# Optimization experiments

Measured on AMD Instinct MI355X. Metric: run time of the kernel, lower is better.

Reference implementation:

```python
import jax, jax.numpy as jnp
import numpy as np


def apply_rotary_emb(x, freqs_cis):
    # x: [B, N, H, Dh], freqs_cis: [N, Dh//2, 2]
    B, N, H, Dh = x.shape
    x2 = x.reshape(B, N, H, Dh // 2, 2)
    f = freqs_cis[None, :, None]  # [1, N, 1, Dh//2, 2]
    real = x2[..., 0] * f[..., 0] - x2[..., 1] * f[..., 1]
    imag = x2[..., 1] * f[..., 0] + x2[..., 0] * f[..., 1]
    out = jnp.stack([real, imag], axis=-1)
    return out.reshape(B, N, H, Dh).astype(x.dtype)


def setup_inputs() -> dict:
    key = jax.random.key(0)
    k1, k2, k3, k4 = jax.random.split(key, 4)
    B, N, dim, n_head = 2, 2048, 2048, 16
    head_dim = dim // n_head
    x = jax.random.normal(k1, (B, N, dim), dtype=jnp.float32)
    # realistic rotary freqs (cos/sin), though random also works for correctness
    pos = jnp.arange(N, dtype=jnp.float32)[:, None]
    inv_freq = 1.0 / (10000.0 ** (jnp.arange(0, head_dim, 2, dtype=jnp.float32) / head_dim))
    ang = pos * inv_freq[None, :]  # [N, Dh//2]
    freqs_cis = jnp.stack([jnp.cos(ang), jnp.sin(ang)], axis=-1)  # [N, Dh//2, 2]
    wqkv = jax.random.normal(k2, (dim, 3 * dim), dtype=jnp.float32) * (dim ** -0.5)
    wo = jax.random.normal(k3, (dim, dim), dtype=jnp.float32) * (dim ** -0.5)
    return {"x": x, "freqs_cis": freqs_cis, "wqkv": wqkv, "wo": wo}


def reference(x, freqs_cis, wqkv, wo):
    B, N, dim = x.shape
    n_head = 16
    head_dim = dim // n_head
    qkv = x @ wqkv  # [B, N, 3*dim]
    q, k, v = jnp.split(qkv, 3, axis=-1)
    q = q.reshape(B, N, n_head, head_dim)
    k = k.reshape(B, N, n_head, head_dim)
    v = v.reshape(B, N, n_head, head_dim)
    q = apply_rotary_emb(q, freqs_cis)
    k = apply_rotary_emb(k, freqs_cis)
    scale = 1.0 / jnp.sqrt(jnp.asarray(head_dim, dtype=q.dtype))
    scores = jnp.einsum('bqhd,bkhd->bhqk', q, k) * scale
    attn = jax.nn.softmax(scores, axis=-1)
    out = jnp.einsum('bhqk,bkhd->bqhd', attn, v).reshape(B, N, dim)
    return out @ wo
```

## Files before the change

kernel.cpp:

```cpp
#include <hip/hip_runtime.h>
#include <hip/hip_bf16.h>
#include <stdint.h>

typedef __attribute__((ext_vector_type(8))) short bf16x8;
typedef __attribute__((ext_vector_type(4))) float f32x4;
typedef __attribute__((ext_vector_type(4))) unsigned short u16x4;
typedef __attribute__((ext_vector_type(8))) unsigned short u16x8;

#define DEV __device__ __forceinline__

DEV unsigned short f2bf(float f) {
  union { __hip_bfloat16 h; unsigned short u; } cv;
  cv.h = __float2bfloat16(f);
  return cv.u;
}

DEV void gload_lds16(const void* g, void* l) {
  __builtin_amdgcn_global_load_lds(
      (__attribute__((address_space(1))) void*)(uintptr_t)g,
      (__attribute__((address_space(3))) void*)(uint32_t)(uintptr_t)l,
      16, 0, 0);
}

__global__ __launch_bounds__(256) void k_convert(const float* __restrict__ in,
                                                 unsigned short* __restrict__ out,
                                                 int n8) {
  int i = blockIdx.x * 256 + threadIdx.x;
  if (i >= n8) return;
  const float4* p = (const float4*)in + (size_t)i * 2;
  float4 a = p[0], b = p[1];
  u16x8 o;
  o[0] = f2bf(a.x); o[1] = f2bf(a.y); o[2] = f2bf(a.z); o[3] = f2bf(a.w);
  o[4] = f2bf(b.x); o[5] = f2bf(b.y); o[6] = f2bf(b.z); o[7] = f2bf(b.w);
  *((u16x8*)out + (size_t)i) = o;
}

__global__ __launch_bounds__(256) void k_transpose_bf16(const float* __restrict__ in,
                                                        unsigned short* __restrict__ out,
                                                        int R, int C) {
  __shared__ float tile[32][33];
  const int t = threadIdx.x;
  const int c0 = blockIdx.x * 32, r0 = blockIdx.y * 32;
  {
    int r = t >> 3, c4 = (t & 7) * 4;
    float4 v = *(const float4*)&in[(size_t)(r0 + r) * C + c0 + c4];
    tile[r][c4] = v.x; tile[r][c4 + 1] = v.y; tile[r][c4 + 2] = v.z; tile[r][c4 + 3] = v.w;
  }
  __syncthreads();
  int c = t >> 3, r4 = (t & 7) * 4;
  u16x4 o;
  o[0] = f2bf(tile[r4 + 0][c]); o[1] = f2bf(tile[r4 + 1][c]);
  o[2] = f2bf(tile[r4 + 2][c]); o[3] = f2bf(tile[r4 + 3][c]);
  *(u16x4*)&out[(size_t)(c0 + c) * R + r0 + r4] = o;
}

template <int EPI>
__global__ __launch_bounds__(256) void k_gemm(
    const unsigned short* __restrict__ A,
    const unsigned short* __restrict__ Bt,
    int Kdim, int Nn,
    float* __restrict__ Cout,
    unsigned short* __restrict__ qb,
    unsigned short* __restrict__ kb,
    unsigned short* __restrict__ vt,
    const float* __restrict__ freqs) {
  __shared__ unsigned short As[128 * 64];
  __shared__ unsigned short Bs[128 * 64];
  const int t = threadIdx.x;
  const int lane = t & 63, wid = t >> 6;
  const int l15 = lane & 15, l4 = lane >> 4;
  const int m0 = blockIdx.y * 128, n0 = blockIdx.x * 128;
  const int wr = (wid >> 1) * 64, wc = (wid & 1) * 64;

  f32x4 acc[4][4];
#pragma unroll
  for (int i = 0; i < 4; i++)
#pragma unroll
    for (int j = 0; j < 4; j++) acc[i][j] = (f32x4)0.f;

  for (int k0 = 0; k0 < Kdim; k0 += 64) {
    __syncthreads();
#pragma unroll
    for (int j = 0; j < 4; j++) {
      int slotbase = j * 256 + wid * 64;
      int slot = slotbase + lane;
      int row = slot >> 3, cc = slot & 7;
      int cg = cc ^ (row & 7);
      gload_lds16(A + (size_t)(m0 + row) * Kdim + k0 + cg * 8, &As[slotbase * 8]);
      gload_lds16(Bt + (size_t)(n0 + row) * Kdim + k0 + cg * 8, &Bs[slotbase * 8]);
    }
    __syncthreads();
#pragma unroll
    for (int kk = 0; kk < 2; kk++) {
      bf16x8 af[4], bfr[4];
#pragma unroll
      for (int mi = 0; mi < 4; mi++) {
        int row = wr + mi * 16 + l15;
        int c = (kk * 4 + l4) ^ (row & 7);
        af[mi] = *(const bf16x8*)&As[row * 64 + c * 8];
      }
#pragma unroll
      for (int ni = 0; ni < 4; ni++) {
        int row = wc + ni * 16 + l15;
        int c = (kk * 4 + l4) ^ (row & 7);
        bfr[ni] = *(const bf16x8*)&Bs[row * 64 + c * 8];
      }
#pragma unroll
      for (int mi = 0; mi < 4; mi++)
#pragma unroll
        for (int ni = 0; ni < 4; ni++)
          acc[mi][ni] = __builtin_amdgcn_mfma_f32_16x16x32_bf16(af[mi], bfr[ni],
                                                                acc[mi][ni], 0, 0, 0);
    }
  }

  if constexpr (EPI == 1) {
#pragma unroll
    for (int mi = 0; mi < 4; mi++) {
      int rowb = m0 + wr + mi * 16 + l4 * 4;
#pragma unroll
      for (int ni = 0; ni < 4; ni++) {
        int col = n0 + wc + ni * 16 + l15;
#pragma unroll
        for (int r = 0; r < 4; r++)
          Cout[(size_t)(rowb + r) * Nn + col] = acc[mi][ni][r];
      }
    }
  } else {
#pragma unroll
    for (int mi = 0; mi < 4; mi++) {
      int rowb = m0 + wr + mi * 16 + l4 * 4;
      int b = rowb >> 11;
      int tok0 = rowb & 2047;
#pragma unroll
      for (int ni = 0; ni < 4; ni++) {
        int col = n0 + wc + ni * 16 + l15;
        int sec = col >> 11;
        int h = (col >> 7) & 15;
        int dh = col & 127;
        if (sec == 2) {
          u16x4 o;
#pragma unroll
          for (int r = 0; r < 4; r++) o[r] = f2bf(acc[mi][ni][r]);
          *(u16x4*)&vt[((size_t)(b * 16 + h) * 128 + dh) * 2048 + tok0] = o;
        } else {
          unsigned short* dst = (sec == 0) ? qb : kb;
          int dh2 = dh >> 1;
          int odd = dh & 1;
#pragma unroll
          for (int r = 0; r < 4; r++) {
            float v = acc[mi][ni][r];
            float p = __shfl_xor(v, 1, 64);
            float2 cs = *(const float2*)&freqs[((size_t)(tok0 + r) * 64 + dh2) * 2];
            float o = odd ? (v * cs.x + p * cs.y) : (v * cs.x - p * cs.y);
            dst[((size_t)(b * 16 + h) * 2048 + tok0 + r) * 128 + dh] = f2bf(o);
          }
        }
      }
    }
  }
}

__global__ __launch_bounds__(256, 2) void k_attn(
    const unsigned short* __restrict__ qb,
    const unsigned short* __restrict__ kb,
    const unsigned short* __restrict__ vt,
    unsigned short* __restrict__ ao) {
  __shared__ unsigned short Ks[2][64 * 128];
  __shared__ unsigned short Vs[2][64 * 128];
  __shared__ unsigned short Ps[4][32 * 64];
  const int t = threadIdx.x;
  const int lane = t & 63, wid = t >> 6;
  const int l15 = lane & 15, l4 = lane >> 4;
  const int qt0 = blockIdx.x * 128;
  const int bh = blockIdx.y;
  const unsigned short* qbase = qb + (size_t)bh * 2048 * 128;
  const unsigned short* kbase = kb + (size_t)bh * 2048 * 128;
  const unsigned short* vbase = vt + (size_t)bh * 128 * 2048;

  bf16x8 qf[2][4];
#pragma unroll
  for (int mi = 0; mi < 2; mi++) {
    int qrow = qt0 + wid * 32 + mi * 16 + l15;
#pragma unroll
    for (int dk = 0; dk < 4; dk++)
      qf[mi][dk] = *(const bf16x8*)&qbase[(size_t)qrow * 128 + dk * 32 + l4 * 8];
  }

  f32x4 O[2][8];
#pragma unroll
  for (int mi = 0; mi < 2; mi++)
#pragma unroll
    for (int df = 0; df < 8; df++) O[mi][df] = (f32x4)0.f;
  float lsum[2][4];
#pragma unroll
  for (int mi = 0; mi < 2; mi++)
#pragma unroll
    for (int r = 0; r < 4; r++) lsum[mi][r] = 0.f;

  const float scale = 0.08838834764831845f;

  auto STAGE = [&](int kv0, int buf) {
#pragma unroll
    for (int j = 0; j < 4; j++) {
      int slotbase = j * 256 + wid * 64;
      int slot = slotbase + lane;
      int rowk = slot >> 4, ck = slot & 15;
      gload_lds16(&kbase[(size_t)(kv0 + rowk) * 128 + (ck ^ (rowk & 7)) * 8],
                  &Ks[buf][slotbase * 8]);
      int rowv = slot >> 3, cv = slot & 7;
      gload_lds16(&vbase[(size_t)rowv * 2048 + kv0 + (cv ^ (rowv & 7)) * 8],
                  &Vs[buf][slotbase * 8]);
    }
  };

  STAGE(0, 0);
  __syncthreads();

  for (int ti = 0; ti < 32; ti++) {
    const int cur = ti & 1;
    if (ti < 31) STAGE((ti + 1) * 64, cur ^ 1);

    f32x4 s[2][4];
#pragma unroll
    for (int mi = 0; mi < 2; mi++)
#pragma unroll
      for (int ni = 0; ni < 4; ni++) s[mi][ni] = (f32x4)0.f;
#pragma unroll
    for (int dk = 0; dk < 4; dk++) {
      bf16x8 kf[4];
#pragma unroll
      for (int ni = 0; ni < 4; ni++) {
        int row = ni * 16 + l15;
        int c = (dk * 4 + l4) ^ (row & 7);
        kf[ni] = *(const bf16x8*)&Ks[cur][row * 128 + c * 8];
      }
#pragma unroll
      for (int mi = 0; mi < 2; mi++)
#pragma unroll
        for (int ni = 0; ni < 4; ni++)
          s[mi][ni] = __builtin_amdgcn_mfma_f32_16x16x32_bf16(qf[mi][dk], kf[ni],
                                                              s[mi][ni], 0, 0, 0);
    }

    unsigned short* pbase = &Ps[wid][0];
#pragma unroll
    for (int mi = 0; mi < 2; mi++)
#pragma unroll
      for (int ni = 0; ni < 4; ni++) {
        int col = ni * 16 + l15;
#pragma unroll
        for (int r = 0; r < 4; r++) {
          float p = __expf(s[mi][ni][r] * scale);
          lsum[mi][r] += p;
          int rowp = mi * 16 + l4 * 4 + r;
          pbase[rowp * 64 + (((col >> 3) ^ (rowp & 7)) << 3) + (col & 7)] = f2bf(p);
        }
      }

    bf16x8 pf[2][2];
#pragma unroll
    for (int mi = 0; mi < 2; mi++)
#pragma unroll
      for (int kk = 0; kk < 2; kk++) {
        int row = mi * 16 + l15;
        int c = (kk * 4 + l4) ^ (row & 7);
        pf[mi][kk] = *(const bf16x8*)&pbase[row * 64 + c * 8];
      }

#pragma unroll
    for (int df = 0; df < 8; df++) {
      bf16x8 vf[2];
#pragma unroll
      for (int kk = 0; kk < 2; kk++) {
        int row = df * 16 + l15;
        int c = (kk * 4 + l4) ^ (row & 7);
        vf[kk] = *(const bf16x8*)&Vs[cur][row * 64 + c * 8];
      }
#pragma unroll
      for (int mi = 0; mi < 2; mi++)
#pragma unroll
        for (int kk = 0; kk < 2; kk++)
          O[mi][df] = __builtin_amdgcn_mfma_f32_16x16x32_bf16(pf[mi][kk], vf[kk],
                                                              O[mi][df], 0, 0, 0);
    }

    __syncthreads();
  }

  float inv[2][4];
#pragma unroll
  for (int mi = 0; mi < 2; mi++)
#pragma unroll
    for (int r = 0; r < 4; r++) {
      float v = lsum[mi][r];
      v += __shfl_xor(v, 1, 64);
      v += __shfl_xor(v, 2, 64);
      v += __shfl_xor(v, 4, 64);
      v += __shfl_xor(v, 8, 64);
      inv[mi][r] = 1.0f / v;
    }

  const int b = bh >> 4, h = bh & 15;
#pragma unroll
  for (int mi = 0; mi < 2; mi++)
#pragma unroll
    for (int df = 0; df < 8; df++)
#pragma unroll
      for (int r = 0; r < 4; r++) {
        int tok = qt0 + wid * 32 + mi * 16 + l4 * 4 + r;
        ao[((size_t)(b * 2048 + tok)) * 2048 + h * 128 + df * 16 + l15] =
            f2bf(O[mi][df][r] * inv[mi][r]);
      }
}

extern "C" void kernel_launch(void* const* d_in, const int* in_sizes, int n_in,
                              void* d_out, int out_size, void* d_ws, size_t ws_size,
                              hipStream_t stream) {
  const float* x     = (const float*)d_in[0];
  const float* freqs = (const float*)d_in[1];
  const float* wqkv  = (const float*)d_in[2];
  const float* wo    = (const float*)d_in[3];
  float* out = (float*)d_out;

  char* ws = (char*)d_ws;
  unsigned short* xb    = (unsigned short*)(ws + 0);
  unsigned short* wqkvT = (unsigned short*)(ws + 16777216);
  unsigned short* woT   = (unsigned short*)(ws + 41943040);
  unsigned short* qb    = (unsigned short*)(ws + 50331648);
  unsigned short* kb    = (unsigned short*)(ws + 67108864);
  unsigned short* vt    = (unsigned short*)(ws + 83886080);
  unsigned short* ao    = (unsigned short*)(ws + 100663296);

  k_convert<<<dim3(4096), dim3(256), 0, stream>>>(x, xb, 1048576);
  k_transpose_bf16<<<dim3(192, 64), dim3(256), 0, stream>>>(wqkv, wqkvT, 2048, 6144);
  k_transpose_bf16<<<dim3(64, 64), dim3(256), 0, stream>>>(wo, woT, 2048, 2048);

  k_gemm<0><<<dim3(48, 32), dim3(256), 0, stream>>>(
      xb, wqkvT, 2048, 6144, nullptr, qb, kb, vt, freqs);

  k_attn<<<dim3(16, 32), dim3(256), 0, stream>>>(qb, kb, vt, ao);

  k_gemm<1><<<dim3(16, 32), dim3(256), 0, stream>>>(
      ao, woT, 2048, 2048, out, nullptr, nullptr, nullptr, nullptr);
}
```

Measured before the change: 287.3 us.

## Rewrite QKV GEMM with 256x256 tiles, double-buffered LDS, and interleaved staging

Splits the templated GEMM into a dedicated QKV kernel using 512-thread blocks with 256x256 output tiles, double-buffered LDS, and global-to-LDS loads interleaved with MFMA quarter-steps behind barriers and raised wave priority. It also remaps block ids so consecutive blocks share tiles for L2 locality. The aim is to hide load latency and raise arithmetic intensity for the largest GEMM. The cost is 128KB of LDS per block and more barriers. The output GEMM is kept as before.

```diff
diff --git a/kernel.cpp b/kernel.cpp
--- a/kernel.cpp
+++ b/kernel.cpp
@@ -54,16 +54,155 @@
   *(u16x4*)&out[(size_t)(c0 + c) * R + r0 + r4] = o;
 }
 
-template <int EPI>
-__global__ __launch_bounds__(256) void k_gemm(
+__global__ __launch_bounds__(512, 2) void k_gemm_qkv(
     const unsigned short* __restrict__ A,
     const unsigned short* __restrict__ Bt,
-    int Kdim, int Nn,
-    float* __restrict__ Cout,
     unsigned short* __restrict__ qb,
     unsigned short* __restrict__ kb,
     unsigned short* __restrict__ vt,
     const float* __restrict__ freqs) {
+  constexpr int Kdim = 2048;
+  __shared__ unsigned short As[2][256 * 64];
+  __shared__ unsigned short Bs[2][256 * 64];
+  const int t = threadIdx.x;
+  const int lane = t & 63, wid = t >> 6;
+  const int l15 = lane & 15, l4 = (lane >> 4) & 3;
+  const int wm = wid >> 2, wn = wid & 3;
+  const int bid = blockIdx.x;
+  const int wg = (bid & 7) * 48 + (bid >> 3);
+  const int by = wg & 15, bx = wg >> 4;
+  const int m0 = by * 256, n0 = bx * 256;
+
+  f32x4 acc[8][4];
+#pragma unroll
+  for (int i = 0; i < 8; i++)
+#pragma unroll
+    for (int j = 0; j < 4; j++) acc[i][j] = (f32x4)0.f;
+
+  auto stageHalf = [&](unsigned short* tile, const unsigned short* src, int half) {
+#pragma unroll
+    for (int cb = 0; cb < 2; cb++) {
+      int slotu = half * 1024 + cb * 512 + wid * 64;
+      int slot = slotu + lane;
+      int row = slot >> 3, cc = slot & 7;
+      int cg = cc ^ (row & 7);
+      gload_lds16(src + (size_t)row * Kdim + cg * 8, tile + slotu * 8);
+    }
+  };
+
+  auto rdA = [&](int buf, int mh, bf16x8 (&f)[4][2]) {
+#pragma unroll
+    for (int mi = 0; mi < 4; mi++) {
+      int row = wm * 128 + mh * 64 + mi * 16 + l15;
+#pragma unroll
+      for (int kk = 0; kk < 2; kk++) {
+        int c = (kk * 4 + l4) ^ (row & 7);
+        f[mi][kk] = *(const bf16x8*)&As[buf][row * 64 + c * 8];
+      }
+    }
+  };
+  auto rdB = [&](int buf, int nh, bf16x8 (&f)[2][2]) {
+#pragma unroll
+    for (int ni = 0; ni < 2; ni++) {
+      int row = wn * 64 + nh * 32 + ni * 16 + l15;
+#pragma unroll
+      for (int kk = 0; kk < 2; kk++) {
+        int c = (kk * 4 + l4) ^ (row & 7);
+        f[ni][kk] = *(const bf16x8*)&Bs[buf][row * 64 + c * 8];
+      }
+    }
+  };
+  auto mmaQ = [&](bf16x8 (&af)[4][2], bf16x8 (&bf)[2][2], int mib, int nib) {
+    __builtin_amdgcn_s_setprio(1);
+#pragma unroll
+    for (int kk = 0; kk < 2; kk++)
+#pragma unroll
+      for (int mi = 0; mi < 4; mi++)
+#pragma unroll
+        for (int ni = 0; ni < 2; ni++)
+          acc[mib + mi][nib + ni] = __builtin_amdgcn_mfma_f32_16x16x32_bf16(
+              af[mi][kk], bf[ni][kk], acc[mib + mi][nib + ni], 0, 0, 0);
+    __builtin_amdgcn_s_setprio(0);
+  };
+
+  const unsigned short* Abase = A + (size_t)m0 * Kdim;
+  const unsigned short* Bbase = Bt + (size_t)n0 * Kdim;
+
+  stageHalf(As[0], Abase, 0);
+  stageHalf(As[0], Abase, 1);
+  stageHalf(Bs[0], Bbase, 0);
+  stageHalf(Bs[0], Bbase, 1);
+  __syncthreads();
+
+  bf16x8 af[4][2], b0[2][2], b1[2][2];
+  for (int j = 0; j < 32; j++) {
+    const int buf = j & 1;
+    const unsigned short* An = Abase + (j + 1) * 64;
+    const unsigned short* Bn = Bbase + (j + 1) * 64;
+    const bool st = (j < 31);
+    rdA(buf, 0, af);
+    rdB(buf, 0, b0);
+    if (st) stageHalf(As[buf ^ 1], An, 0);
+    __builtin_amdgcn_s_barrier();
+    asm volatile("s_waitcnt lgkmcnt(0)" ::: "memory");
+    mmaQ(af, b0, 0, 0);
+    __builtin_amdgcn_s_barrier();
+    rdB(buf, 1, b1);
+    if (st) stageHalf(As[buf ^ 1], An, 1);
+    __builtin_amdgcn_s_barrier();
+    asm volatile("s_waitcnt lgkmcnt(0)" ::: "memory");
+    mmaQ(af, b1, 0, 2);
+    __builtin_amdgcn_s_barrier();
+    rdA(buf, 1, af);
+    if (st) stageHalf(Bs[buf ^ 1], Bn, 0);
+    __builtin_amdgcn_s_barrier();
+    asm volatile("s_waitcnt lgkmcnt(0)" ::: "memory");
+    mmaQ(af, b0, 4, 0);
+    __builtin_amdgcn_s_barrier();
+    if (st) stageHalf(Bs[buf ^ 1], Bn, 1);
+    __builtin_amdgcn_s_barrier();
+    mmaQ(af, b1, 4, 2);
+    __syncthreads();
+  }
+
+#pragma unroll
+  for (int mi = 0; mi < 8; mi++) {
+    int rowb = m0 + wm * 128 + mi * 16 + l4 * 4;
+    int b = rowb >> 11;
+    int tok0 = rowb & 2047;
+#pragma unroll
+    for (int ni = 0; ni < 4; ni++) {
+      int col = n0 + wn * 64 + ni * 16 + l15;
+      int sec = col >> 11;
+      int h = (col >> 7) & 15;
+      int dh = col & 127;
+      if (sec == 2) {
+        u16x4 o;
+#pragma unroll
+        for (int r = 0; r < 4; r++) o[r] = f2bf(acc[mi][ni][r]);
+        *(u16x4*)&vt[((size_t)(b * 16 + h) * 128 + dh) * 2048 + tok0] = o;
+      } else {
+        unsigned short* dst = (sec == 0) ? qb : kb;
+        int dh2 = dh >> 1;
+        int odd = dh & 1;
+#pragma unroll
+        for (int r = 0; r < 4; r++) {
+          float v = acc[mi][ni][r];
+          float p = __shfl_xor(v, 1, 64);
+          float2 cs = *(const float2*)&freqs[((size_t)(tok0 + r) * 64 + dh2) * 2];
+          float o = odd ? (v * cs.x + p * cs.y) : (v * cs.x - p * cs.y);
+          dst[((size_t)(b * 16 + h) * 2048 + tok0 + r) * 128 + dh] = f2bf(o);
+        }
+      }
+    }
+  }
+}
+
+__global__ __launch_bounds__(256) void k_gemm_out(
+    const unsigned short* __restrict__ A,
+    const unsigned short* __restrict__ Bt,
+    int Kdim, int Nn,
+    float* __restrict__ Cout) {
   __shared__ unsigned short As[128 * 64];
   __shared__ unsigned short Bs[128 * 64];
   const int t = threadIdx.x;
@@ -114,49 +253,15 @@
     }
   }
 
-  if constexpr (EPI == 1) {
-#pragma unroll
-    for (int mi = 0; mi < 4; mi++) {
-      int rowb = m0 + wr + mi * 16 + l4 * 4;
-#pragma unroll
-      for (int ni = 0; ni < 4; ni++) {
-        int col = n0 + wc + ni * 16 + l15;
-#pragma unroll
-        for (int r = 0; r < 4; r++)
-          Cout[(size_t)(rowb + r) * Nn + col] = acc[mi][ni][r];
-      }
-    }
-  } else {
-#pragma unroll
-    for (int mi = 0; mi < 4; mi++) {
-      int rowb = m0 + wr + mi * 16 + l4 * 4;
-      int b = rowb >> 11;
-      int tok0 = rowb & 2047;
-#pragma unroll
-      for (int ni = 0; ni < 4; ni++) {
-        int col = n0 + wc + ni * 16 + l15;
-        int sec = col >> 11;
-        int h = (col >> 7) & 15;
-        int dh = col & 127;
-        if (sec == 2) {
-          u16x4 o;
-#pragma unroll
-          for (int r = 0; r < 4; r++) o[r] = f2bf(acc[mi][ni][r]);
-          *(u16x4*)&vt[((size_t)(b * 16 + h) * 128 + dh) * 2048 + tok0] = o;
-        } else {
-          unsigned short* dst = (sec == 0) ? qb : kb;
-          int dh2 = dh >> 1;
-          int odd = dh & 1;
-#pragma unroll
-          for (int r = 0; r < 4; r++) {
-            float v = acc[mi][ni][r];
-            float p = __shfl_xor(v, 1, 64);
-            float2 cs = *(const float2*)&freqs[((size_t)(tok0 + r) * 64 + dh2) * 2];
-            float o = odd ? (v * cs.x + p * cs.y) : (v * cs.x - p * cs.y);
-            dst[((size_t)(b * 16 + h) * 2048 + tok0 + r) * 128 + dh] = f2bf(o);
-          }
-        }
-      }
+#pragma unroll
+  for (int mi = 0; mi < 4; mi++) {
+    int rowb = m0 + wr + mi * 16 + l4 * 4;
+#pragma unroll
+    for (int ni = 0; ni < 4; ni++) {
+      int col = n0 + wc + ni * 16 + l15;
+#pragma unroll
+      for (int r = 0; r < 4; r++)
+        Cout[(size_t)(rowb + r) * Nn + col] = acc[mi][ni][r];
     }
   }
 }
@@ -336,11 +441,9 @@
   k_transpose_bf16<<<dim3(192, 64), dim3(256), 0, stream>>>(wqkv, wqkvT, 2048, 6144);
   k_transpose_bf16<<<dim3(64, 64), dim3(256), 0, stream>>>(wo, woT, 2048, 2048);
 
-  k_gemm<0><<<dim3(48, 32), dim3(256), 0, stream>>>(
-      xb, wqkvT, 2048, 6144, nullptr, qb, kb, vt, freqs);
+  k_gemm_qkv<<<dim3(384), dim3(512), 0, stream>>>(xb, wqkvT, qb, kb, vt, freqs);
 
   k_attn<<<dim3(16, 32), dim3(256), 0, stream>>>(qb, kb, vt, ao);
 
-  k_gemm<1><<<dim3(16, 32), dim3(256), 0, stream>>>(
-      ao, woT, 2048, 2048, out, nullptr, nullptr, nullptr, nullptr);
-}
+  k_gemm_out<<<dim3(16, 32), dim3(256), 0, stream>>>(ao, woT, 2048, 2048, out);
+}
```

After: 283.3 us. About the same (-1.4%).
